# Kernel tuning notes

Measured on AMD Instinct MI355X. Metric: run time of the kernel, lower is better.

## Reference

```python
import jax, jax.numpy as jnp
import numpy as np

KS = 2       # kernel_size (pad (0,1,0,1)+unfold only tiles to HxW for k=2)
L = 2        # num_attn_blocks
NH = 4       # n_heads
C = 128      # latent_dim
DH = C // NH
SCALE = 1.0 / float(np.sqrt(DH))


def _ln(x, eps=1e-6):
    m = jnp.mean(x, axis=-1, keepdims=True)
    v = jnp.var(x, axis=-1, keepdims=True)
    return (x - m) * jax.lax.rsqrt(v + eps)


def setup_inputs() -> dict:
    key = jax.random.key(0)
    ks = jax.random.split(key, 24)
    B, Hd, Wd, upf = 2, 64, 96, 2
    d = {
        'feat_map': jax.random.normal(ks[0], (B, C, Hd, Wd), jnp.float32),
        'feat_map_up': jax.random.normal(ks[1], (B, C, Hd * upf, Wd * upf), jnp.float32),
    }
    shapes = {'ctx_ln_b': (L, C), 'q_w': (L, C, C), 'q_b': (L, C), 'k_w': (L, C, C), 'k_b': (L, C),
              'v_w': (L, C, C), 'v_b': (L, C), 'o_w': (L, C, C), 'o_b': (L, C),
              'fc1_w': (L, C, 4 * C), 'fc1_b': (L, 4 * C), 'fc2_w': (L, 4 * C, C), 'fc2_b': (L, C),
              'out1_w': (3 * C, 3 * C), 'out1_b': (3 * C,), 'out2_w': (3 * C, 1), 'out2_b': (1,)}
    for i, (n, shp) in enumerate(shapes.items()):
        d[n] = jax.random.normal(ks[2 + i], shp, jnp.float32) * 0.02
    d['ctx_ln_g'] = jnp.ones((L, C), jnp.float32)
    d['upsample_factor'] = 2
    return d


def _forward(feat_map, feat_map_up, ctx_ln_g, ctx_ln_b, q_w, q_b, k_w, k_b, v_w, v_b,
             o_w, o_b, fc1_w, fc1_b, fc2_w, fc2_b, out1_w, out1_b, out2_w, out2_b, upf):
    B, _, Hd, Wd = feat_map.shape
    Hu, Wu = Hd * upf, Wd * upf
    N, K2 = B * Hu * Wu, KS * KS
    rh = jnp.minimum((jnp.arange(Hu) // upf)[:, None] + jnp.arange(KS)[None, :], Hd - 1)  # (Hu,KS)
    rw = jnp.minimum((jnp.arange(Wu) // upf)[:, None] + jnp.arange(KS)[None, :], Wd - 1)  # (Wu,KS)
    ctx = feat_map[:, :, rh][:, :, :, :, rw]                      # (B,C,Hu,KS,Wu,KS)
    ctx = jnp.transpose(ctx, (0, 2, 4, 3, 5, 1)).reshape(N, K2, C)  # (N,K2,C)
    # ALiBi bias: -L1(|up pixel coord - upf*down window coord|), separable in y/x
    dy = -jnp.abs(jnp.arange(Hu)[:, None] - rh * upf).astype(jnp.float32)  # (Hu,KS)
    dx = -jnp.abs(jnp.arange(Wu)[:, None] - rw * upf).astype(jnp.float32)  # (Wu,KS)
    cd = (dy[:, None, :, None] + dx[None, :, None, :]).reshape(Hu * Wu, K2)
    cd = jnp.tile(cd, (B, 1))                                     # (N,K2)
    x24 = 24.0 ** (1.0 / NH)
    slopes = 1.0 / x24 ** (jnp.arange(NH, dtype=jnp.float32) + 1.0)
    bias = slopes[None, :, None, None] * cd[:, None, None, :]     # (N,NH,1,K2)

    x = jnp.transpose(feat_map_up, (0, 2, 3, 1)).reshape(N, 1, C)
    for l in range(L):
        xn = _ln(x)
        cn = _ln(ctx, eps=1e-5) * ctx_ln_g[l] + ctx_ln_b[l]
        q = (xn @ q_w[l] + q_b[l]).reshape(N, 1, NH, DH).transpose(0, 2, 1, 3)
        k = (cn @ k_w[l] + k_b[l]).reshape(N, K2, NH, DH).transpose(0, 2, 1, 3)
        v = (cn @ v_w[l] + v_b[l]).reshape(N, K2, NH, DH).transpose(0, 2, 1, 3)
        sim = jnp.einsum('nhqd,nhkd->nhqk', q, k) * SCALE + bias
        attn = jax.nn.softmax(sim, axis=-1)
        o = jnp.einsum('nhqk,nhkd->nhqd', attn, v).transpose(0, 2, 1, 3).reshape(N, 1, C)
        x = x + o @ o_w[l] + o_b[l]
        h = _ln(x)
        x = x + jax.nn.gelu(h @ fc1_w[l] + fc1_b[l], approximate=True) @ fc2_w[l] + fc2_b[l]

    xf = _ln(x)      # (N,1,C)
    cf = _ln(ctx)    # (N,K2,C)
    fin = jnp.concatenate([jnp.broadcast_to(xf, (N, K2, C)), cf, xf - cf], axis=-1)  # (N,K2,3C)
    h1 = jax.nn.gelu(fin @ out1_w + out1_b, approximate=False)
    out = (h1 @ out2_w + out2_b).reshape(B, Hu, Wu, K2).transpose(0, 3, 1, 2)  # (B,K2,Hu,Wu)
    return jax.nn.softmax(out, axis=1)


def reference(feat_map, feat_map_up, ctx_ln_b, q_w, q_b, k_w, k_b, v_w, v_b, o_w, o_b,
              fc1_w, fc1_b, fc2_w, fc2_b, out1_w, out1_b, out2_w, out2_b, ctx_ln_g,
              upsample_factor):
    return _forward(feat_map, feat_map_up, ctx_ln_g, ctx_ln_b, q_w, q_b, k_w, k_b,
                    v_w, v_b, o_w, o_b, fc1_w, fc1_b, fc2_w, fc2_b,
                    out1_w, out1_b, out2_w, out2_b, upsample_factor)
```

## Files before the change

### kernel.cpp

```cpp
#include <hip/hip_runtime.h>
#include <math.h>

#define C_   128
#define HU_  128
#define WU_  192
#define HD_  64
#define WD_  96
#define HWD_ (HD_ * WD_)

typedef unsigned short u16;
typedef __attribute__((ext_vector_type(8))) short s8v;
typedef __attribute__((ext_vector_type(4))) float f4v;

#define OFF_Q   0
#define OFF_K   32768
#define OFF_V   65536
#define OFF_O   98304
#define OFF_F1  131072
#define OFF_F2  262144
#define OFF_XC  393216
#define OFF_CC  442368
#define OFF_NRM 491520
#define OFF_VB  2064384

#define SLOT 2176

__device__ __forceinline__ u16 f2bf(float f) {
    unsigned u = __float_as_uint(f);
    unsigned r = (u + 0x7FFFu + ((u >> 16) & 1u)) >> 16;
    return (u16)r;
}
__device__ __forceinline__ float bfu(u16 h) { return __uint_as_float(((unsigned)h) << 16); }

__device__ __forceinline__ float gelu_tanh(float x) {
    float u = 1.5957691216057308f * (x + 0.044715f * x * x * x);
    float e = __expf(u);
    float th = 1.0f - 2.0f / (1.0f + e);
    return 0.5f * x * (1.0f + th);
}
__device__ __forceinline__ float fast_erf(float x) {
    float z = fabsf(x);
    float t = 1.0f / (1.0f + 0.3275911f * z);
    float p = t * (0.254829592f + t * (-0.284496736f + t * (1.421413741f +
              t * (-1.453152027f + t * 1.061405429f))));
    float r = 1.0f - p * __expf(-z * z);
    return copysignf(r, x);
}
__device__ __forceinline__ float gelu_erf(float x) {
    return 0.5f * x * (1.0f + fast_erf(x * 0.7071067811865476f));
}

__device__ __forceinline__ void glds1(const u16* src, u16* dst, int lane) {
    __builtin_amdgcn_global_load_lds(
        (const __attribute__((address_space(1))) void*)(src + (size_t)lane * 8),
        (__attribute__((address_space(3))) void*)dst, 16, 0, 0);
}
#define GW2() do { asm volatile("s_waitcnt vmcnt(2)" ::: "memory"); __builtin_amdgcn_s_barrier(); } while (0)
#define GW0() do { asm volatile("s_waitcnt vmcnt(0)" ::: "memory"); __builtin_amdgcn_s_barrier(); } while (0)
#define BAR() __builtin_amdgcn_s_barrier()
#define WFENCE() asm volatile("s_waitcnt lgkmcnt(0)" ::: "memory")

__global__ __launch_bounds__(256) void swz_all(
    const float* __restrict__ q_w, const float* __restrict__ k_w,
    const float* __restrict__ v_w, const float* __restrict__ o_w,
    const float* __restrict__ f1w, const float* __restrict__ f2w,
    const float* __restrict__ o1w,
    const float* __restrict__ ctx_g, const float* __restrict__ ctx_b,
    const float* __restrict__ vb_in, u16* __restrict__ ws)
{
    int tid = blockIdx.x * 256 + threadIdx.x;
    int f = tid >> 6, lane = tid & 63;
    if (f >= 964) return;
    if (f >= 960) {
        int lf = f - 960;
        int ly = lf >> 1, col = (lf & 1) * 64 + lane;
        float s = vb_in[ly * 128 + col];
        const float* bp = ctx_b + ly * 128;
        const float* wp = v_w + (size_t)ly * 128 * 128 + col;
        for (int c = 0; c < 128; ++c) s += bp[c] * wp[(size_t)c * 128];
        ((float*)(ws + OFF_VB))[ly * 128 + col] = s;
        return;
    }
    int rq = 8 * (lane >> 4), cq = lane & 15;
    const float* src; const float* src2 = nullptr; float sgn = 1.f;
    int NT, N, dstoff, lf;
    bool scale_g = false;
    if (f < 64)       { src = q_w;  NT = 8;  N = 128; dstoff = OFF_Q;  lf = f; }
    else if (f < 128) { src = k_w;  NT = 8;  N = 128; dstoff = OFF_K;  lf = f - 64;  scale_g = true; }
    else if (f < 192) { src = v_w;  NT = 8;  N = 128; dstoff = OFF_V;  lf = f - 128; scale_g = true; }
    else if (f < 256) { src = o_w;  NT = 8;  N = 128; dstoff = OFF_O;  lf = f - 192; }
    else if (f < 512) { src = f1w;  NT = 32; N = 512; dstoff = OFF_F1; lf = f - 256; }
    else if (f < 768) { src = f2w;  NT = 8;  N = 128; dstoff = OFF_F2; lf = f - 512; }
    else if (f < 864) { src = o1w;             src2 = o1w + 256 * 384; sgn =  1.f;
                        NT = 24; N = 384; dstoff = OFF_XC; lf = f - 768; }
    else              { src = o1w + 128 * 384; src2 = o1w + 256 * 384; sgn = -1.f;
                        NT = 24; N = 384; dstoff = OFF_CC; lf = f - 864; }
    int kt = lf / NT, nt = lf - kt * NT;
    int row0 = kt * 32 + rq, col = nt * 16 + cq;
    s8v o;
#pragma unroll
    for (int j = 0; j < 8; ++j) {
        float v = src[(size_t)(row0 + j) * N + col];
        if (src2) v += sgn * src2[(size_t)(row0 + j) * N + col];
        if (scale_g) v *= ctx_g[row0 + j];
        o[j] = (short)f2bf(v);
    }
    *(s8v*)(ws + dstoff + (size_t)lf * 512 + (size_t)lane * 8) = o;
}

__global__ __launch_bounds__(256) void norm_kernel(const float* __restrict__ fm,
                                                   u16* __restrict__ dst) {
    int row = blockIdx.x;
    int b = row >> 6, y = row & 63;
    __shared__ float tile[128 * 97];
    __shared__ float smean[96], srst[96];
    for (int idx = threadIdx.x; idx < 128 * 96; idx += 256) {
        int c = idx / 96, w = idx - c * 96;
        tile[c * 97 + w] = fm[(((size_t)b * 128 + c) * 64 + y) * 96 + w];
    }
    __syncthreads();
    if (threadIdx.x < 96) {
        int w = threadIdx.x;
        float s = 0.f, ss = 0.f;
        for (int c = 0; c < 128; ++c) { float v = tile[c * 97 + w]; s += v; ss += v * v; }
        float mn = s * (1.f / 128.f);
        smean[w] = mn;
        srst[w]  = rsqrtf(ss * (1.f / 128.f) - mn * mn + 1e-5f);
    }
    __syncthreads();
    for (int idx = threadIdx.x; idx < 96 * 16; idx += 256) {
        int w = idx >> 4, cg = idx & 15;
        float mn = smean[w], iv = srst[w];
        s8v o;
#pragma unroll
        for (int j = 0; j < 8; ++j)
            o[j] = (short)f2bf((tile[(8 * cg + j) * 97 + w] - mn) * iv);
        *(s8v*)(dst + ((size_t)row * 96 + w) * 128 + 8 * cg) = o;
    }
}

__global__ __launch_bounds__(256, 2) void fused_kernel(
    const u16*  __restrict__ nrmb, const float* __restrict__ fmu,
    const u16*  __restrict__ wsb,
    const float* __restrict__ qb, const float* __restrict__ ob,
    const float* __restrict__ f1b, const float* __restrict__ f2b,
    const float* __restrict__ o1b, const float* __restrict__ o2w,
    const float* __restrict__ o2b,
    float* __restrict__ out)
{
    const int tid  = threadIdx.x;
    const int wid  = tid >> 6;
    const int lane = tid & 63;
    const int cidx = lane & 15, quad = lane >> 4;
    const int n0 = blockIdx.x * 64 + wid * 16;
    const int b  = n0 / (HU_ * WU_);
    const int rem = n0 - b * (HU_ * WU_);
    const int hu  = rem / WU_;
    const int wu0 = rem - hu * WU_;

    __shared__ __align__(16) u16 wlds[2][4096];
    __shared__ __align__(16) u16 arena2[4][2 * SLOT];
    u16*   const arena = arena2[wid];
    float* const s_at  = (float*)(arena + SLOT + 1024);
    float* const s_rs  = s_at;

    const float* vbp = (const float*)(wsb + OFF_VB);

    float xacc[8][4];
#pragma unroll
    for (int nt = 0; nt < 8; ++nt) {
        int ch = 16 * nt + cidx;
        float4 v = *(const float4*)(fmu + ((size_t)(b * C_ + ch) * HU_ + hu) * WU_ + wu0 + 4 * quad);
        xacc[nt][0] = v.x; xacc[nt][1] = v.y; xacc[nt][2] = v.z; xacc[nt][3] = v.w;
    }

    const float slopes[4] = {0.451801007f, 0.204124145f, 0.092223264f, 0.041666668f};
    const int ry0 = min(hu >> 1, HD_ - 1);
    const int ry1 = min((hu >> 1) + 1, HD_ - 1);
    const float dyv0 = -(float)abs(hu - 2 * ry0);
    const float dyv1 = -(float)abs(hu - 2 * ry1);

    const int k2l = cidx & 3;
    const int ryl = (k2l >> 1) ? ry1 : ry0;
    int cbase[4];
#pragma unroll
    for (int mt = 0; mt < 4; ++mt) {
        int p = 4 * mt + (cidx >> 2);
        int rxv = min(((wu0 + p) >> 1) + (k2l & 1), WD_ - 1);
        cbase[mt] = ((b * HD_ + ryl) * WD_ + rxv) * 128;
    }

#pragma unroll 1
    for (int ly = 0; ly < 2; ++ly) {
        const u16* Wq = wsb + OFF_Q  + ly * 16384;
        const u16* Wk = wsb + OFF_K  + ly * 16384;
        const u16* Wv = wsb + OFF_V  + ly * 16384;
        const u16* Wo = wsb + OFF_O  + ly * 16384;
        const u16* W1 = wsb + OFF_F1 + ly * 65536;
        const u16* W2 = wsb + OFF_F2 + ly * 65536;

        s8v fr[4][2];

#pragma unroll
        for (int jl = 0; jl < 2; ++jl) {
            int j = 2 * wid + jl;
            glds1(Wq + (size_t)j * 512, &wlds[0][j * 512], lane);
        }
#pragma unroll
        for (int jl = 0; jl < 2; ++jl) {
            int j = 2 * wid + jl;
            glds1(Wq + (size_t)(8 + j) * 512, &wlds[1][j * 512], lane);
        }

        {
            float mo[4], io[4];
#pragma unroll
            for (int r = 0; r < 4; ++r) {
                float s = 0.f, ss = 0.f;
#pragma unroll
                for (int nt = 0; nt < 8; ++nt) { float v = xacc[nt][r]; s += v; ss += v * v; }
#pragma unroll
                for (int m = 1; m <= 8; m <<= 1) { s += __shfl_xor(s, m, 64); ss += __shfl_xor(ss, m, 64); }
                float mn = s * (1.f / 128.f);
                mo[r] = mn; io[r] = rsqrtf(ss * (1.f / 128.f) - mn * mn + 1e-6f);
            }
#pragma unroll
            for (int nt = 0; nt < 8; ++nt)
#pragma unroll
                for (int r = 0; r < 4; ++r)
                    arena[(4 * quad + r) * 136 + 16 * nt + cidx] =
                        f2bf((xacc[nt][r] - mo[r]) * io[r]);
        }
        WFENCE();
        s8v a_xn[4];
#pragma unroll
        for (int kt = 0; kt < 4; ++kt)
            a_xn[kt] = *(const s8v*)(arena + cidx * 136 + kt * 32 + 8 * quad);

        {
            f4v qa[8];
#pragma unroll
            for (int nt = 0; nt < 8; ++nt) {
                float bvv = qb[ly * C_ + 16 * nt + cidx];
                f4v t = {bvv, bvv, bvv, bvv}; qa[nt] = t;
            }
#pragma unroll
            for (int g = 0; g < 4; ++g) {
                if (g < 3) { GW2(); } else { GW0(); }
#pragma unroll
                for (int nt = 0; nt < 8; ++nt) {
                    s8v w = *(const s8v*)&wlds[g & 1][nt * 512 + lane * 8];
                    qa[nt] = __builtin_amdgcn_mfma_f32_16x16x32_bf16(a_xn[g], w, qa[nt], 0, 0, 0);
                }
                BAR();
                if (g < 2) {
#pragma unroll
                    for (int jl = 0; jl < 2; ++jl) {
                        int j = 2 * wid + jl;
                        glds1(Wq + (size_t)((g + 2) * 8 + j) * 512, &wlds[g & 1][j * 512], lane);
                    }
                }
            }
#pragma unroll
            for (int kt = 0; kt < 4; ++kt)
#pragma unroll
                for (int i = 0; i < 2; ++i)
                    fr[kt][i] = *(const s8v*)(nrmb + cbase[i] + kt * 32 + 8 * quad);
#pragma unroll
            for (int jl = 0; jl < 2; ++jl) {
                int j = 2 * wid + jl;
                glds1(Wk + (size_t)(((j & 3) * 8) + (j >> 2)) * 512, &wlds[0][j * 512], lane);
            }
#pragma unroll
            for (int jl = 0; jl < 2; ++jl) {
                int j = 2 * wid + jl;
                int jc = 8 + j;
                glds1(Wk + (size_t)(((jc & 3) * 8) + (jc >> 2)) * 512, &wlds[1][j * 512], lane);
            }
#pragma unroll
            for (int nt = 0; nt < 8; ++nt)
#pragma unroll
                for (int r = 0; r < 4; ++r)
                    arena[(4 * quad + r) * 136 + 16 * nt + cidx] = f2bf(qa[nt][r]);
        }
        WFENCE();

#pragma unroll
        for (int g = 0; g < 8; ++g) {
            if (g < 7) { GW2(); } else { GW0(); }
            const int mh = g >> 2, h = g & 3;
            float part[2][4];
#pragma unroll
            for (int i = 0; i < 2; ++i)
#pragma unroll
                for (int r = 0; r < 4; ++r) part[i][r] = 0.f;
#pragma unroll
            for (int ntp = 0; ntp < 2; ++ntp) {
                const int nt = 2 * h + ntp;
                f4v ka[2];
#pragma unroll
                for (int i = 0; i < 2; ++i) { f4v t = {0.f, 0.f, 0.f, 0.f}; ka[i] = t; }
#pragma unroll
                for (int kt = 0; kt < 4; ++kt) {
                    s8v w = *(const s8v*)&wlds[g & 1][(ntp * 4 + kt) * 512 + lane * 8];
                    ka[0] = __builtin_amdgcn_mfma_f32_16x16x32_bf16(fr[kt][0], w, ka[0], 0, 0, 0);
                    ka[1] = __builtin_amdgcn_mfma_f32_16x16x32_bf16(fr[kt][1], w, ka[1], 0, 0, 0);
                }
#pragma unroll
                for (int i = 0; i < 2; ++i) {
                    float qv = bfu(arena[(4 * (2 * mh + i) + quad) * 136 + 16 * nt + cidx]);
#pragma unroll
                    for (int r = 0; r < 4; ++r) part[i][r] = fmaf(qv, ka[i][r], part[i][r]);
                }
            }
#pragma unroll
            for (int i = 0; i < 2; ++i)
#pragma unroll
                for (int r = 0; r < 4; ++r) {
#pragma unroll
                    for (int m = 1; m <= 8; m <<= 1) part[i][r] += __shfl_xor(part[i][r], m, 64);
                }
            if (cidx == 0) {
#pragma unroll
                for (int i = 0; i < 2; ++i) {
                    float4 t = {part[i][0], part[i][1], part[i][2], part[i][3]};
                    *(float4*)&s_at[(4 * (2 * mh + i) + quad) * 16 + 4 * h] = t;
                }
            }
            BAR();
            if (g == 2) {
#pragma unroll
                for (int kt = 0; kt < 4; ++kt)
#pragma unroll
                    for (int i = 0; i < 2; ++i)
                        fr[kt][i] = *(const s8v*)(nrmb + cbase[2 + i] + kt * 32 + 8 * quad);
            }
            if (g < 6) {
                const int gn = g + 2;
#pragma unroll
                for (int jl = 0; jl < 2; ++jl) {
                    int j = 2 * wid + jl;
                    int jc = 8 * (gn & 3) + j;
                    glds1(Wk + (size_t)(((jc & 3) * 8) + (jc >> 2)) * 512, &wlds[g & 1][j * 512], lane);
                }
            }
        }
#pragma unroll
        for (int kt = 0; kt < 4; ++kt)
#pragma unroll
            for (int i = 0; i < 2; ++i)
                fr[kt][i] = *(const s8v*)(nrmb + cbase[i] + kt * 32 + 8 * quad);
#pragma unroll
        for (int jl = 0; jl < 2; ++jl) {
            int j = 2 * wid + jl;
            glds1(Wv + (size_t)(((j & 3) * 8) + (j >> 2)) * 512, &wlds[0][j * 512], lane);
        }
#pragma unroll
        for (int jl = 0; jl < 2; ++jl) {
            int j = 2 * wid + jl;
            glds1(Wv + (size_t)(((j & 3) * 8) + 2 + (j >> 2)) * 512, &wlds[1][j * 512], lane);
        }
        WFENCE();

        {
            int p = lane >> 2, h = lane & 3;
            float4 sc = *(float4*)&s_at[p * 16 + 4 * h];
            int pw = wu0 + p;
            float sim[4] = {sc.x, sc.y, sc.z, sc.w};
#pragma unroll
            for (int r = 0; r < 4; ++r) {
                int rxv = min((pw >> 1) + (r & 1), WD_ - 1);
                float cd = ((r >> 1) ? dyv1 : dyv0) - (float)abs(pw - 2 * rxv);
                sim[r] = sim[r] * 0.17677669529663687f + slopes[h] * cd;
            }
            float mx = fmaxf(fmaxf(sim[0], sim[1]), fmaxf(sim[2], sim[3]));
            float e0 = __expf(sim[0] - mx), e1 = __expf(sim[1] - mx);
            float e2 = __expf(sim[2] - mx), e3 = __expf(sim[3] - mx);
            float si = 1.f / (e0 + e1 + e2 + e3);
            float4 at = {e0 * si, e1 * si, e2 * si, e3 * si};
            *(float4*)&s_at[p * 16 + 4 * h] = at;
        }
        WFENCE();

#pragma unroll
        for (int g = 0; g < 8; ++g) {
            if (g < 7) { GW2(); } else { GW0(); }
            const int mh = g >> 2, gp = g & 3;
#pragma unroll
            for (int ntp = 0; ntp < 2; ++ntp) {
                const int nt = 2 * gp + ntp;
                float vbb = vbp[ly * C_ + 16 * nt + cidx];
                f4v va[2];
#pragma unroll
                for (int i = 0; i < 2; ++i) { f4v t = {vbb, vbb, vbb, vbb}; va[i] = t; }
#pragma unroll
                for (int kt = 0; kt < 4; ++kt) {
                    s8v w = *(const s8v*)&wlds[g & 1][(ntp * 4 + kt) * 512 + lane * 8];
                    va[0] = __builtin_amdgcn_mfma_f32_16x16x32_bf16(fr[kt][0], w, va[0], 0, 0, 0);
                    va[1] = __builtin_amdgcn_mfma_f32_16x16x32_bf16(fr[kt][1], w, va[1], 0, 0, 0);
                }
                const int h = nt >> 1;
#pragma unroll
                for (int i = 0; i < 2; ++i) {
                    const int mt = 2 * mh + i;
                    float4 at = *(float4*)&s_at[(4 * mt + quad) * 16 + 4 * h];
                    float ov = at.x * va[i][0] + at.y * va[i][1] + at.z * va[i][2] + at.w * va[i][3];
                    arena[(4 * mt + quad) * 136 + 16 * nt + cidx] = f2bf(ov);
                }
            }
            BAR();
            if (g == 2) {
#pragma unroll
                for (int kt = 0; kt < 4; ++kt)
#pragma unroll
                    for (int i = 0; i < 2; ++i)
                        fr[kt][i] = *(const s8v*)(nrmb + cbase[2 + i] + kt * 32 + 8 * quad);
            }
            if (g < 6) {
                const int gq = (g + 2) & 3;
#pragma unroll
                for (int jl = 0; jl < 2; ++jl) {
                    int j = 2 * wid + jl;
                    glds1(Wv + (size_t)(((j & 3) * 8) + 2 * gq + (j >> 2)) * 512, &wlds[g & 1][j * 512], lane);
                }
            }
        }
#pragma unroll
        for (int jl = 0; jl < 2; ++jl) {
            int j = 2 * wid + jl;
            glds1(Wo + (size_t)j * 512, &wlds[0][j * 512], lane);
        }
#pragma unroll
        for (int jl = 0; jl < 2; ++jl) {
            int j = 2 * wid + jl;
            glds1(Wo + (size_t)(8 + j) * 512, &wlds[1][j * 512], lane);
        }
        WFENCE();

        {
            s8v a_o[4];
#pragma unroll
            for (int kt = 0; kt < 4; ++kt)
                a_o[kt] = *(const s8v*)(arena + cidx * 136 + kt * 32 + 8 * quad);
            f4v oa[8];
#pragma unroll
            for (int nt = 0; nt < 8; ++nt) {
                float bvv = ob[ly * C_ + 16 * nt + cidx];
                f4v t = {bvv, bvv, bvv, bvv}; oa[nt] = t;
            }
#pragma unroll
            for (int g = 0; g < 4; ++g) {
                if (g < 3) { GW2(); } else { GW0(); }
#pragma unroll
                for (int nt = 0; nt < 8; ++nt) {
                    s8v w = *(const s8v*)&wlds[g & 1][nt * 512 + lane * 8];
                    oa[nt] = __builtin_amdgcn_mfma_f32_16x16x32_bf16(a_o[g], w, oa[nt], 0, 0, 0);
                }
                BAR();
                if (g < 2) {
#pragma unroll
                    for (int jl = 0; jl < 2; ++jl) {
                        int j = 2 * wid + jl;
                        glds1(Wo + (size_t)((g + 2) * 8 + j) * 512, &wlds[g & 1][j * 512], lane);
                    }
                }
            }
#pragma unroll
            for (int jl = 0; jl < 2; ++jl) {
                int j = 2 * wid + jl;
                glds1(W1 + (size_t)j * 512, &wlds[0][j * 512], lane);
            }
#pragma unroll
            for (int jl = 0; jl < 2; ++jl) {
                int j = 2 * wid + jl;
                glds1(W1 + (size_t)(32 + j) * 512, &wlds[1][j * 512], lane);
            }
#pragma unroll
            for (int nt = 0; nt < 8; ++nt)
#pragma unroll
                for (int r = 0; r < 4; ++r) xacc[nt][r] += oa[nt][r];
        }

        {
            float mo[4], io[4];
#pragma unroll
            for (int r = 0; r < 4; ++r) {
                float s = 0.f, ss = 0.f;
#pragma unroll
                for (int nt = 0; nt < 8; ++nt) { float v = xacc[nt][r]; s += v; ss += v * v; }
#pragma unroll
                for (int m = 1; m <= 8; m <<= 1) { s += __shfl_xor(s, m, 64); ss += __shfl_xor(ss, m, 64); }
                float mn = s * (1.f / 128.f);
                mo[r] = mn; io[r] = rsqrtf(ss * (1.f / 128.f) - mn * mn + 1e-6f);
            }
#pragma unroll
            for (int nt = 0; nt < 8; ++nt)
#pragma unroll
                for (int r = 0; r < 4; ++r)
                    arena[(4 * quad + r) * 136 + 16 * nt + cidx] =
                        f2bf((xacc[nt][r] - mo[r]) * io[r]);
        }
        WFENCE();
        s8v a_hn[4];
#pragma unroll
        for (int kt = 0; kt < 4; ++kt)
            a_hn[kt] = *(const s8v*)(arena + cidx * 136 + kt * 32 + 8 * quad);

        {
            f4v ga[8];
#pragma unroll
            for (int nt = 0; nt < 8; ++nt) {
                float bvv = f2b[ly * C_ + 16 * nt + cidx];
                f4v t = {bvv, bvv, bvv, bvv}; ga[nt] = t;
            }
#pragma unroll 1
            for (int c = 0; c < 4; ++c) {
                f4v fa[8];
#pragma unroll
                for (int nt = 0; nt < 8; ++nt) {
                    float bvv = f1b[ly * 512 + 128 * c + 16 * nt + cidx];
                    f4v t = {bvv, bvv, bvv, bvv}; fa[nt] = t;
                }
#pragma unroll
                for (int g = 0; g < 4; ++g) {
                    if (g < 3) { GW2(); } else { GW0(); }
#pragma unroll
                    for (int nt = 0; nt < 8; ++nt) {
                        s8v w = *(const s8v*)&wlds[g & 1][nt * 512 + lane * 8];
                        fa[nt] = __builtin_amdgcn_mfma_f32_16x16x32_bf16(a_hn[g], w, fa[nt], 0, 0, 0);
                    }
                    BAR();
                    if (g < 2) {
#pragma unroll
                        for (int jl = 0; jl < 2; ++jl) {
                            int j = 2 * wid + jl;
                            glds1(W1 + (size_t)((g + 2) * 32 + 8 * c + j) * 512, &wlds[g & 1][j * 512], lane);
                        }
                    }
                }
#pragma unroll
                for (int jl = 0; jl < 2; ++jl) {
                    int j = 2 * wid + jl;
                    glds1(W2 + (size_t)(32 * c + j) * 512, &wlds[0][j * 512], lane);
                }
#pragma unroll
                for (int jl = 0; jl < 2; ++jl) {
                    int j = 2 * wid + jl;
                    glds1(W2 + (size_t)(32 * c + 8 + j) * 512, &wlds[1][j * 512], lane);
                }
#pragma unroll
                for (int nt = 0; nt < 8; ++nt)
#pragma unroll
                    for (int r = 0; r < 4; ++r)
                        arena[SLOT + (4 * quad + r) * 136 + 16 * nt + cidx] =
                            f2bf(gelu_tanh(fa[nt][r]));
                WFENCE();
#pragma unroll
                for (int g = 0; g < 4; ++g) {
                    if (g < 3) { GW2(); } else { GW0(); }
                    s8v a = *(const s8v*)(arena + SLOT + cidx * 136 + g * 32 + 8 * quad);
#pragma unroll
                    for (int nt = 0; nt < 8; ++nt) {
                        s8v w = *(const s8v*)&wlds[g & 1][nt * 512 + lane * 8];
                        ga[nt] = __builtin_amdgcn_mfma_f32_16x16x32_bf16(a, w, ga[nt], 0, 0, 0);
                    }
                    BAR();
                    if (g < 2) {
#pragma unroll
                        for (int jl = 0; jl < 2; ++jl) {
                            int j = 2 * wid + jl;
                            glds1(W2 + (size_t)(32 * c + (g + 2) * 8 + j) * 512, &wlds[g & 1][j * 512], lane);
                        }
                    }
                }
                if (c < 3) {
#pragma unroll
                    for (int jl = 0; jl < 2; ++jl) {
                        int j = 2 * wid + jl;
                        glds1(W1 + (size_t)(8 * (c + 1) + j) * 512, &wlds[0][j * 512], lane);
                    }
#pragma unroll
                    for (int jl = 0; jl < 2; ++jl) {
                        int j = 2 * wid + jl;
                        glds1(W1 + (size_t)(32 + 8 * (c + 1) + j) * 512, &wlds[1][j * 512], lane);
                    }
                }
            }
#pragma unroll
            for (int nt = 0; nt < 8; ++nt)
#pragma unroll
                for (int r = 0; r < 4; ++r) xacc[nt][r] += ga[nt][r];
        }
    }

    const u16* Wxc = wsb + OFF_XC;
    const u16* Wcc = wsb + OFF_CC;
#pragma unroll
    for (int jl = 0; jl < 3; ++jl) {
        int j = 3 * wid + jl;
        glds1(Wxc + (size_t)((j / 3) * 24 + (j % 3)) * 512, &wlds[j / 6][(j % 6) * 512], lane);
    }
    {
        float mo[4], io[4];
#pragma unroll
        for (int r = 0; r < 4; ++r) {
            float s = 0.f, ss = 0.f;
#pragma unroll
            for (int nt = 0; nt < 8; ++nt) { float v = xacc[nt][r]; s += v; ss += v * v; }
#pragma unroll
            for (int m = 1; m <= 8; m <<= 1) { s += __shfl_xor(s, m, 64); ss += __shfl_xor(ss, m, 64); }
            float mn = s * (1.f / 128.f);
            mo[r] = mn; io[r] = rsqrtf(ss * (1.f / 128.f) - mn * mn + 1e-6f);
        }
#pragma unroll
        for (int nt = 0; nt < 8; ++nt)
#pragma unroll
            for (int r = 0; r < 4; ++r)
                arena[(4 * quad + r) * 136 + 16 * nt + cidx] =
                    f2bf((xacc[nt][r] - mo[r]) * io[r]);
    }
    WFENCE();
    s8v a_xf[4];
#pragma unroll
    for (int kt = 0; kt < 4; ++kt)
        a_xf[kt] = *(const s8v*)(arena + cidx * 136 + kt * 32 + 8 * quad);

    float part[4][4];
#pragma unroll
    for (int mt = 0; mt < 4; ++mt)
#pragma unroll
        for (int r = 0; r < 4; ++r) part[mt][r] = 0.f;

#pragma unroll 1
    for (int it = 0; it < 8; ++it) {
        const int nbase = 6 * (it >> 1) + 3 * (it & 1);
        {
            f4v hx[3];
#pragma unroll
            for (int ntl = 0; ntl < 3; ++ntl) {
                float hb = o1b[16 * (nbase + ntl) + cidx];
                f4v t = {hb, hb, hb, hb}; hx[ntl] = t;
            }
            if (wid < 2) { asm volatile("s_waitcnt vmcnt(0)" ::: "memory"); }
            BAR();
#pragma unroll
            for (int kt = 0; kt < 2; ++kt)
#pragma unroll
                for (int ntl = 0; ntl < 3; ++ntl) {
                    s8v w = *(const s8v*)&wlds[0][(kt * 3 + ntl) * 512 + lane * 8];
                    hx[ntl] = __builtin_amdgcn_mfma_f32_16x16x32_bf16(a_xf[kt], w, hx[ntl], 0, 0, 0);
                }
            if (wid >= 2) { asm volatile("s_waitcnt vmcnt(0)" ::: "memory"); }
            BAR();
#pragma unroll
            for (int kt = 2; kt < 4; ++kt)
#pragma unroll
                for (int ntl = 0; ntl < 3; ++ntl) {
                    s8v w = *(const s8v*)&wlds[1][((kt - 2) * 3 + ntl) * 512 + lane * 8];
                    hx[ntl] = __builtin_amdgcn_mfma_f32_16x16x32_bf16(a_xf[kt], w, hx[ntl], 0, 0, 0);
                }
            BAR();
            if (it < 7) {
                const int nb2 = 6 * ((it + 1) >> 1) + 3 * ((it + 1) & 1);
#pragma unroll
                for (int jl = 0; jl < 3; ++jl) {
                    int j = 3 * wid + jl;
                    glds1(Wxc + (size_t)((j / 3) * 24 + nb2 + (j % 3)) * 512, &wlds[j / 6][(j % 6) * 512], lane);
                }
            }
#pragma unroll
            for (int ntl = 0; ntl < 3; ++ntl)
#pragma unroll
                for (int r = 0; r < 4; ++r)
                    arena[SLOT + (4 * quad + r) * 56 + 16 * ntl + cidx] = f2bf(hx[ntl][r]);
        }
        WFENCE();

        f4v hc[3][4];
#pragma unroll
        for (int ntl = 0; ntl < 3; ++ntl)
#pragma unroll
            for (int mt = 0; mt < 4; ++mt) { f4v t = {0.f, 0.f, 0.f, 0.f}; hc[ntl][mt] = t; }
#pragma unroll 1
        for (int kt = 0; kt < 4; ++kt) {
            s8v frh[4];
#pragma unroll
            for (int mt = 0; mt < 4; ++mt)
                frh[mt] = *(const s8v*)(nrmb + cbase[mt] + kt * 32 + 8 * quad);
#pragma unroll
            for (int ntl = 0; ntl < 3; ++ntl) {
                s8v w = *(const s8v*)(Wcc + ((size_t)((kt * 24 + nbase + ntl) * 64 + lane)) * 8);
#pragma unroll
                for (int mt = 0; mt < 4; ++mt)
                    hc[ntl][mt] = __builtin_amdgcn_mfma_f32_16x16x32_bf16(frh[mt], w, hc[ntl][mt], 0, 0, 0);
            }
        }

#pragma unroll
        for (int ntl = 0; ntl < 3; ++ntl) {
            float w2v = o2w[16 * (nbase + ntl) + cidx];
#pragma unroll
            for (int mt = 0; mt < 4; ++mt)
#pragma unroll
                for (int r = 0; r < 4; ++r) {
                    float h1 = hc[ntl][mt][r] +
                               bfu(arena[SLOT + (4 * mt + quad) * 56 + 16 * ntl + cidx]);
                    part[mt][r] = fmaf(gelu_erf(h1), w2v, part[mt][r]);
                }
        }
        WFENCE();
    }

#pragma unroll
    for (int mt = 0; mt < 4; ++mt)
#pragma unroll
        for (int r = 0; r < 4; ++r) {
#pragma unroll
            for (int m = 1; m <= 8; m <<= 1) part[mt][r] += __shfl_xor(part[mt][r], m, 64);
            part[mt][r] += o2b[0];
        }
    if (cidx == 0) {
#pragma unroll
        for (int mt = 0; mt < 4; ++mt) {
            float4 t = {part[mt][0], part[mt][1], part[mt][2], part[mt][3]};
            *(float4*)&s_rs[(4 * mt + quad) * 4] = t;
        }
    }
    WFENCE();

    if (lane < 16) {
        int p = lane;
        float4 vv = *(float4*)&s_rs[4 * p];
        float mx = fmaxf(fmaxf(vv.x, vv.y), fmaxf(vv.z, vv.w));
        float e0 = __expf(vv.x - mx), e1 = __expf(vv.y - mx);
        float e2 = __expf(vv.z - mx), e3 = __expf(vv.w - mx);
        float si = 1.f / (e0 + e1 + e2 + e3);
        size_t base = ((size_t)(b * 4) * HU_ + hu) * WU_ + wu0 + p;
        out[base]                          = e0 * si;
        out[base + (size_t)HU_ * WU_]      = e1 * si;
        out[base + (size_t)2 * HU_ * WU_]  = e2 * si;
        out[base + (size_t)3 * HU_ * WU_]  = e3 * si;
    }
}

extern "C" void kernel_launch(void* const* d_in, const int* in_sizes, int n_in,
                              void* d_out, int out_size, void* d_ws, size_t ws_size,
                              hipStream_t stream) {
    const float* feat_map    = (const float*)d_in[0];
    const float* feat_map_up = (const float*)d_in[1];
    const float* ctx_ln_b    = (const float*)d_in[2];
    const float* q_w  = (const float*)d_in[3];
    const float* q_b  = (const float*)d_in[4];
    const float* k_w  = (const float*)d_in[5];
    const float* v_w  = (const float*)d_in[7];
    const float* v_b  = (const float*)d_in[8];
    const float* o_w  = (const float*)d_in[9];
    const float* o_b  = (const float*)d_in[10];
    const float* fc1_w = (const float*)d_in[11];
    const float* fc1_b = (const float*)d_in[12];
    const float* fc2_w = (const float*)d_in[13];
    const float* fc2_b = (const float*)d_in[14];
    const float* out1_w = (const float*)d_in[15];
    const float* out1_b = (const float*)d_in[16];
    const float* out2_w = (const float*)d_in[17];
    const float* out2_b = (const float*)d_in[18];
    const float* ctx_ln_g = (const float*)d_in[19];
    float* out = (float*)d_out;
    u16* ws = (u16*)d_ws;

    swz_all<<<242, 256, 0, stream>>>(q_w, k_w, v_w, o_w, fc1_w, fc2_w, out1_w,
                                     ctx_ln_g, ctx_ln_b, v_b, ws);
    norm_kernel<<<128, 256, 0, stream>>>(feat_map, ws + OFF_NRM);

    fused_kernel<<<768, 256, 0, stream>>>(
        ws + OFF_NRM, feat_map_up, ws,
        q_b, o_b, fc1_b, fc2_b,
        out1_b, out2_w, out2_b, out);
}
```

Measured before the change: 407.5 us.

## Merge prologue kernels, use packed bf16 conversion, and tweak unrolling

Folds the weight-swizzle kernel and the per-row LayerNorm kernel into one launch by giving the extra blocks the normalization work, which removes one kernel launch. Replaces scalar float-to-bf16 rounding in the fused kernel with the v_cvt_pk_bf16_f32 instruction, which converts two values at once. Hoists the attention-weight LDS reads out of the inner loop of the output projection. Raises unroll factors on the bias fold loop and the context GEMM loop, which may add register pressure under the 2-block occupancy bound.

```diff
diff --git a/kernel.cpp b/kernel.cpp
--- a/kernel.cpp
+++ b/kernel.cpp
@@ -31,6 +31,13 @@
     return (u16)r;
 }
 __device__ __forceinline__ float bfu(u16 h) { return __uint_as_float(((unsigned)h) << 16); }
+
+__device__ __forceinline__ void st2bf(u16* p0, u16* p1, float a, float b) {
+    unsigned r;
+    asm("v_cvt_pk_bf16_f32 %0, %1, %2" : "=v"(r) : "v"(a), "v"(b));
+    *p0 = (u16)r;
+    *p1 = (u16)(r >> 16);
+}
 
 __device__ __forceinline__ float gelu_tanh(float x) {
     float u = 1.5957691216057308f * (x + 0.044715f * x * x * x);
@@ -60,14 +67,47 @@
 #define BAR() __builtin_amdgcn_s_barrier()
 #define WFENCE() asm volatile("s_waitcnt lgkmcnt(0)" ::: "memory")
 
-__global__ __launch_bounds__(256) void swz_all(
+__global__ __launch_bounds__(256) void prologue_all(
     const float* __restrict__ q_w, const float* __restrict__ k_w,
     const float* __restrict__ v_w, const float* __restrict__ o_w,
     const float* __restrict__ f1w, const float* __restrict__ f2w,
     const float* __restrict__ o1w,
     const float* __restrict__ ctx_g, const float* __restrict__ ctx_b,
-    const float* __restrict__ vb_in, u16* __restrict__ ws)
+    const float* __restrict__ vb_in, const float* __restrict__ fm,
+    u16* __restrict__ ws)
 {
+    if (blockIdx.x >= 242) {
+        int row = blockIdx.x - 242;
+        int b = row >> 6, y = row & 63;
+        __shared__ float tile[128 * 97];
+        __shared__ float smean[96], srst[96];
+        u16* dst = ws + OFF_NRM;
+        for (int idx = threadIdx.x; idx < 128 * 96; idx += 256) {
+            int c = idx / 96, w = idx - c * 96;
+            tile[c * 97 + w] = fm[(((size_t)b * 128 + c) * 64 + y) * 96 + w];
+        }
+        __syncthreads();
+        if (threadIdx.x < 96) {
+            int w = threadIdx.x;
+            float s = 0.f, ss = 0.f;
+            for (int c = 0; c < 128; ++c) { float v = tile[c * 97 + w]; s += v; ss += v * v; }
+            float mn = s * (1.f / 128.f);
+            smean[w] = mn;
+            srst[w]  = rsqrtf(ss * (1.f / 128.f) - mn * mn + 1e-5f);
+        }
+        __syncthreads();
+        for (int idx = threadIdx.x; idx < 96 * 16; idx += 256) {
+            int w = idx >> 4, cg = idx & 15;
+            float mn = smean[w], iv = srst[w];
+            s8v o;
+#pragma unroll
+            for (int j = 0; j < 8; ++j)
+                o[j] = (short)f2bf((tile[(8 * cg + j) * 97 + w] - mn) * iv);
+            *(s8v*)(dst + ((size_t)row * 96 + w) * 128 + 8 * cg) = o;
+        }
+        return;
+    }
+
     int tid = blockIdx.x * 256 + threadIdx.x;
     int f = tid >> 6, lane = tid & 63;
     if (f >= 964) return;
@@ -77,6 +117,7 @@
         float s = vb_in[ly * 128 + col];
         const float* bp = ctx_b + ly * 128;
         const float* wp = v_w + (size_t)ly * 128 * 128 + col;
+#pragma unroll 8
         for (int c = 0; c < 128; ++c) s += bp[c] * wp[(size_t)c * 128];
         ((float*)(ws + OFF_VB))[ly * 128 + col] = s;
         return;
@@ -106,37 +147,6 @@
         o[j] = (short)f2bf(v);
     }
     *(s8v*)(ws + dstoff + (size_t)lf * 512 + (size_t)lane * 8) = o;
-}
-
-__global__ __launch_bounds__(256) void norm_kernel(const float* __restrict__ fm,
-                                                   u16* __restrict__ dst) {
-    int row = blockIdx.x;
-    int b = row >> 6, y = row & 63;
-    __shared__ float tile[128 * 97];
-    __shared__ float smean[96], srst[96];
-    for (int idx = threadIdx.x; idx < 128 * 96; idx += 256) {
-        int c = idx / 96, w = idx - c * 96;
-        tile[c * 97 + w] = fm[(((size_t)b * 128 + c) * 64 + y) * 96 + w];
-    }
-    __syncthreads();
-    if (threadIdx.x < 96) {
-        int w = threadIdx.x;
-        float s = 0.f, ss = 0.f;
-        for (int c = 0; c < 128; ++c) { float v = tile[c * 97 + w]; s += v; ss += v * v; }
-        float mn = s * (1.f / 128.f);
-        smean[w] = mn;
-        srst[w]  = rsqrtf(ss * (1.f / 128.f) - mn * mn + 1e-5f);
-    }
-    __syncthreads();
-    for (int idx = threadIdx.x; idx < 96 * 16; idx += 256) {
-        int w = idx >> 4, cg = idx & 15;
-        float mn = smean[w], iv = srst[w];
-        s8v o;
-#pragma unroll
-        for (int j = 0; j < 8; ++j)
-            o[j] = (short)f2bf((tile[(8 * cg + j) * 97 + w] - mn) * iv);
-        *(s8v*)(dst + ((size_t)row * 96 + w) * 128 + 8 * cg) = o;
-    }
 }
 
 __global__ __launch_bounds__(256, 2) void fused_kernel(
@@ -227,9 +237,11 @@
 #pragma unroll
             for (int nt = 0; nt < 8; ++nt)
 #pragma unroll
-                for (int r = 0; r < 4; ++r)
-                    arena[(4 * quad + r) * 136 + 16 * nt + cidx] =
-                        f2bf((xacc[nt][r] - mo[r]) * io[r]);
+                for (int r = 0; r < 4; r += 2)
+                    st2bf(arena + (4 * quad + r) * 136 + 16 * nt + cidx,
+                          arena + (4 * quad + r + 1) * 136 + 16 * nt + cidx,
+                          (xacc[nt][r] - mo[r]) * io[r],
+                          (xacc[nt][r + 1] - mo[r + 1]) * io[r + 1]);
         }
         WFENCE();
         s8v a_xn[4];
@@ -280,8 +292,10 @@
 #pragma unroll
             for (int nt = 0; nt < 8; ++nt)
 #pragma unroll
-                for (int r = 0; r < 4; ++r)
-                    arena[(4 * quad + r) * 136 + 16 * nt + cidx] = f2bf(qa[nt][r]);
+                for (int r = 0; r < 4; r += 2)
+                    st2bf(arena + (4 * quad + r) * 136 + 16 * nt + cidx,
+                          arena + (4 * quad + r + 1) * 136 + 16 * nt + cidx,
+                          qa[nt][r], qa[nt][r + 1]);
         }
         WFENCE();
 
@@ -386,6 +400,9 @@
         for (int g = 0; g < 8; ++g) {
             if (g < 7) { GW2(); } else { GW0(); }
             const int mh = g >> 2, gp = g & 3;
+            float4 at0 = *(float4*)&s_at[(4 * (2 * mh + 0) + quad) * 16 + 4 * gp];
+            float4 at1 = *(float4*)&s_at[(4 * (2 * mh + 1) + quad) * 16 + 4 * gp];
+            float ov[2][2];
 #pragma unroll
             for (int ntp = 0; ntp < 2; ++ntp) {
                 const int nt = 2 * gp + ntp;
@@ -399,14 +416,15 @@
                     va[0] = __builtin_amdgcn_mfma_f32_16x16x32_bf16(fr[kt][0], w, va[0], 0, 0, 0);
                     va[1] = __builtin_amdgcn_mfma_f32_16x16x32_bf16(fr[kt][1], w, va[1], 0, 0, 0);
                 }
-                const int h = nt >> 1;
-#pragma unroll
-                for (int i = 0; i < 2; ++i) {
-                    const int mt = 2 * mh + i;
-                    float4 at = *(float4*)&s_at[(4 * mt + quad) * 16 + 4 * h];
-                    float ov = at.x * va[i][0] + at.y * va[i][1] + at.z * va[i][2] + at.w * va[i][3];
-                    arena[(4 * mt + quad) * 136 + 16 * nt + cidx] = f2bf(ov);
-                }
+                ov[ntp][0] = at0.x * va[0][0] + at0.y * va[0][1] + at0.z * va[0][2] + at0.w * va[0][3];
+                ov[ntp][1] = at1.x * va[1][0] + at1.y * va[1][1] + at1.z * va[1][2] + at1.w * va[1][3];
+            }
+#pragma unroll
+            for (int i = 0; i < 2; ++i) {
+                const int mt = 2 * mh + i;
+                st2bf(arena + (4 * mt + quad) * 136 + 16 * (2 * gp) + cidx,
+                      arena + (4 * mt + quad) * 136 + 16 * (2 * gp + 1) + cidx,
+                      ov[0][i], ov[1][i]);
             }
             BAR();
             if (g == 2) {
@@ -496,9 +514,11 @@
 #pragma unroll
             for (int nt = 0; nt < 8; ++nt)
 #pragma unroll
-                for (int r = 0; r < 4; ++r)
-                    arena[(4 * quad + r) * 136 + 16 * nt + cidx] =
-                        f2bf((xacc[nt][r] - mo[r]) * io[r]);
+                for (int r = 0; r < 4; r += 2)
+                    st2bf(arena + (4 * quad + r) * 136 + 16 * nt + cidx,
+                          arena + (4 * quad + r + 1) * 136 + 16 * nt + cidx,
+                          (xacc[nt][r] - mo[r]) * io[r],
+                          (xacc[nt][r + 1] - mo[r + 1]) * io[r + 1]);
         }
         WFENCE();
         s8v a_hn[4];
@@ -551,9 +571,10 @@
 #pragma unroll
                 for (int nt = 0; nt < 8; ++nt)
 #pragma unroll
-                    for (int r = 0; r < 4; ++r)
-                        arena[SLOT + (4 * quad + r) * 136 + 16 * nt + cidx] =
-                            f2bf(gelu_tanh(fa[nt][r]));
+                    for (int r = 0; r < 4; r += 2)
+                        st2bf(arena + SLOT + (4 * quad + r) * 136 + 16 * nt + cidx,
+                              arena + SLOT + (4 * quad + r + 1) * 136 + 16 * nt + cidx,
+                              gelu_tanh(fa[nt][r]), gelu_tanh(fa[nt][r + 1]));
                 WFENCE();
 #pragma unroll
                 for (int g = 0; g < 4; ++g) {
@@ -615,9 +636,11 @@
 #pragma unroll
         for (int nt = 0; nt < 8; ++nt)
 #pragma unroll
-            for (int r = 0; r < 4; ++r)
-                arena[(4 * quad + r) * 136 + 16 * nt + cidx] =
-                    f2bf((xacc[nt][r] - mo[r]) * io[r]);
+            for (int r = 0; r < 4; r += 2)
+                st2bf(arena + (4 * quad + r) * 136 + 16 * nt + cidx,
+                      arena + (4 * quad + r + 1) * 136 + 16 * nt + cidx,
+                      (xacc[nt][r] - mo[r]) * io[r],
+                      (xacc[nt][r + 1] - mo[r + 1]) * io[r + 1]);
     }
     WFENCE();
     s8v a_xf[4];
@@ -671,8 +694,10 @@
 #pragma unroll
             for (int ntl = 0; ntl < 3; ++ntl)
 #pragma unroll
-                for (int r = 0; r < 4; ++r)
-                    arena[SLOT + (4 * quad + r) * 56 + 16 * ntl + cidx] = f2bf(hx[ntl][r]);
+                for (int r = 0; r < 4; r += 2)
+                    st2bf(arena + SLOT + (4 * quad + r) * 56 + 16 * ntl + cidx,
+                          arena + SLOT + (4 * quad + r + 1) * 56 + 16 * ntl + cidx,
+                          hx[ntl][r], hx[ntl][r + 1]);
         }
         WFENCE();
 
@@ -681,7 +706,7 @@
         for (int ntl = 0; ntl < 3; ++ntl)
 #pragma unroll
             for (int mt = 0; mt < 4; ++mt) { f4v t = {0.f, 0.f, 0.f, 0.f}; hc[ntl][mt] = t; }
-#pragma unroll 1
+#pragma unroll 2
         for (int kt = 0; kt < 4; ++kt) {
             s8v frh[4];
 #pragma unroll
@@ -768,9 +793,8 @@
     float* out = (float*)d_out;
     u16* ws = (u16*)d_ws;
 
-    swz_all<<<242, 256, 0, stream>>>(q_w, k_w, v_w, o_w, fc1_w, fc2_w, out1_w,
-                                     ctx_ln_g, ctx_ln_b, v_b, ws);
-    norm_kernel<<<128, 256, 0, stream>>>(feat_map, ws + OFF_NRM);
+    prologue_all<<<370, 256, 0, stream>>>(q_w, k_w, v_w, o_w, fc1_w, fc2_w, out1_w,
+                                          ctx_ln_g, ctx_ln_b, v_b, feat_map, ws);
 
     fused_kernel<<<768, 256, 0, stream>>>(
         ws + OFF_NRM, feat_map_up, ws,
```

After: 390.1 us. 1.04x faster.
